# Kernel optimization log

Hardware: AMD Instinct MI355X
Metric: run time of the kernel (lower is better)

## Reference

```python
import jax, jax.numpy as jnp
import numpy as np

B, T, IN = 4, 1024, 172
D, H, FF, L, NCLS = 512, 8, 2048, 8, 1296
HD = D // H
EPS = 1e-5


def setup_inputs() -> dict:
    key = jax.random.key(0)
    ks = jax.random.split(key, 16)
    rn = lambda k, s, sc=0.02: jax.random.normal(k, s, jnp.float32) * sc
    return {
        "poses": jax.random.normal(ks[0], (B, T, IN), jnp.float32),
        "pose_w": rn(ks[1], (D, IN)), "pose_b": jnp.zeros((D,), jnp.float32),
        "in_w": rn(ks[2], (L, 3 * D, D)), "in_b": jnp.zeros((L, 3 * D), jnp.float32),
        "out_w": rn(ks[3], (L, D, D)), "out_b": jnp.zeros((L, D), jnp.float32),
        "ln1_g": jnp.ones((L, D), jnp.float32), "ln1_b": jnp.zeros((L, D), jnp.float32),
        "ffn_w1": rn(ks[4], (L, FF, D)), "ffn_b1": jnp.zeros((L, FF), jnp.float32),
        "ffn_w2": rn(ks[5], (L, D, FF)), "ffn_b2": jnp.zeros((L, D), jnp.float32),
        "ln2_g": jnp.ones((L, D), jnp.float32), "ln2_b": jnp.zeros((L, D), jnp.float32),
        "tcn1_w": rn(ks[6], (512, D, 5)), "tcn1_b": jnp.zeros((512,), jnp.float32),
        "tcn2_w": rn(ks[7], (D, 512, 5)), "tcn2_b": jnp.zeros((D,), jnp.float32),
        "fc1_w": rn(ks[8], (128, D)), "fc1_b": jnp.zeros((128,), jnp.float32),
        "fc2_w": rn(ks[9], (NCLS, 128)), "fc2_b": jnp.zeros((NCLS,), jnp.float32),
    }


def _pos_enc(seq_len, d):
    # PositionalEncoding1D: interleaved sin/cos per frequency pair
    inv_freq = 1.0 / (10000.0 ** (jnp.arange(0, d, 2, dtype=jnp.float32) / d))
    ang = jnp.arange(seq_len, dtype=jnp.float32)[:, None] * inv_freq  # [T, d/2]
    return jnp.stack([jnp.sin(ang), jnp.cos(ang)], axis=-1).reshape(seq_len, d)


def _ln(x, g, b):
    m = x.mean(-1, keepdims=True)
    v = jnp.var(x, axis=-1, keepdims=True)
    return (x - m) * jax.lax.rsqrt(v + EPS) * g + b


def _encoder_layer(x, iw, ib, ow, ob, g1, b1, w1, c1, w2, c2, g2, b2):
    # post-norm TransformerEncoderLayer, eager (non-flash) attention
    Bc, Tc, _ = x.shape
    qkv = x @ iw.T + ib                       # [B,T,3D]
    q, k, v = jnp.split(qkv, 3, axis=-1)
    q = q.reshape(Bc, Tc, H, HD)
    k = k.reshape(Bc, Tc, H, HD)
    v = v.reshape(Bc, Tc, H, HD)
    scores = jnp.einsum('bqhd,bkhd->bhqk', q, k) / jnp.sqrt(jnp.float32(HD))
    attn = jax.nn.softmax(scores, axis=-1)    # explicit weights (need_weights=True)
    o = jnp.einsum('bhqk,bkhd->bqhd', attn, v).reshape(Bc, Tc, D)
    o = o @ ow.T + ob
    x = _ln(x + o, g1, b1)
    f = jax.nn.relu(x @ w1.T + c1) @ w2.T + c2
    return _ln(x + f, g2, b2)


def _conv1d(x, w, b):  # x [B,T,C_in], w [C_out,C_in,5], pad=2
    y = jax.lax.conv_general_dilated(
        x.transpose(0, 2, 1), w, window_strides=(1,), padding=((2, 2),),
        dimension_numbers=('NCH', 'OIH', 'NCH'))
    return y.transpose(0, 2, 1) + b


def _avgpool2(x):  # kernel=2 stride=2 along time
    Bc, Tc, C = x.shape
    return x.reshape(Bc, Tc // 2, 2, C).mean(axis=2)


def reference(poses, pose_w, pose_b, in_w, in_b, out_w, out_b, ln1_g, ln1_b,
              ffn_w1, ffn_b1, ffn_w2, ffn_b2, ln2_g, ln2_b,
              tcn1_w, tcn1_b, tcn2_w, tcn2_b, fc1_w, fc1_b, fc2_w, fc2_b):
    x = poses.reshape(poses.shape[0], poses.shape[1], -1) @ pose_w.T + pose_b
    x = x + _pos_enc(x.shape[1], D)[None]

    def run_stack(h, idx):
        for i in idx:
            h = _encoder_layer(h, in_w[i], in_b[i], out_w[i], out_b[i],
                               ln1_g[i], ln1_b[i], ffn_w1[i], ffn_b1[i],
                               ffn_w2[i], ffn_b2[i], ln2_g[i], ln2_b[i])
        return h

    h = run_stack(x, (0, 1))
    h = run_stack(h, (2, 3)) + h
    h = run_stack(h, (4, 5)) + h
    h = run_stack(h, (6, 7)) + h

    h = _avgpool2(h)                 # [B,T/2,D]
    h = _conv1d(h, tcn1_w, tcn1_b)   # [B,T/2,512]
    h = _avgpool2(h)                 # [B,T/4,512]
    h = _conv1d(h, tcn2_w, tcn2_b)   # [B,T/4,D]
    h = h @ fc1_w.T + fc1_b
    logits = h @ fc2_w.T + fc2_b     # [B,T/4,num_classes]
    return logits
```

## Files before the change

kernel.cpp:

```cpp
#include <hip/hip_runtime.h>
#include <hip/hip_bf16.h>

static constexpr int kB = 4;
static constexpr int kT = 1024;
static constexpr int kIn = 172;
static constexpr int kD = 512;
static constexpr int kH = 8;
static constexpr int kHD = 64;
static constexpr int kFF = 2048;
static constexpr int kNCLS = 1296;
static constexpr float kEps = 1e-5f;

typedef __attribute__((ext_vector_type(8))) short bf16x8_t;
typedef __attribute__((ext_vector_type(4))) float f32x4_t;
typedef __attribute__((ext_vector_type(8))) unsigned short u16x8_t;
typedef __attribute__((ext_vector_type(4))) unsigned short u16x4_t;

static __device__ __forceinline__ unsigned short f2bf(float f) {
  unsigned int u = __float_as_uint(f);
  unsigned int r = (u + 0x7fffu + ((u >> 16) & 1u)) >> 16;
  return (unsigned short)r;
}

__global__ void cvt_kernel(const float* __restrict__ src, ushort* __restrict__ dst, int n8)
{
  const int i = blockIdx.x * 256 + threadIdx.x;
  if (i >= n8) return;
  const float4 a = *(const float4*)&src[i * 8];
  const float4 b = *(const float4*)&src[i * 8 + 4];
  u16x8_t t;
  t[0] = f2bf(a.x); t[1] = f2bf(a.y); t[2] = f2bf(a.z); t[3] = f2bf(a.w);
  t[4] = f2bf(b.x); t[5] = f2bf(b.y); t[6] = f2bf(b.z); t[7] = f2bf(b.w);
  *(u16x8_t*)&dst[i * 8] = t;
}

template<int MR, int NR, int WM, int WN>
__global__ __launch_bounds__(WM * WN * 64) void bgemm_kernel(
    const ushort* __restrict__ A, const ushort* __restrict__ W,
    const float* __restrict__ bias, const float* __restrict__ resid,
    float* __restrict__ C, ushort* __restrict__ Cb, int M, int N, int K, int doRelu)
{
  constexpr int THREADS = WM * WN * 64;
  constexpr int BM = MR * 16 * WM, BN = NR * 16 * WN;
  constexpr int SRD = 72;
  constexpr int TPRA = THREADS / BM, CSA = 64 / TPRA, NLA = CSA / 8;
  constexpr int TPRB = THREADS / BN, CSB = 64 / TPRB, NLB = CSB / 8;
  __shared__ ushort As[BM * SRD];
  __shared__ ushort Bs[BN * SRD];

  const int tid = threadIdx.x;
  int bid = blockIdx.y * gridDim.x + blockIdx.x;
  const int nwg = gridDim.x * gridDim.y;
  if ((nwg & 7) == 0) bid = (bid & 7) * (nwg >> 3) + (bid >> 3);
  const int bm = (bid / gridDim.x) * BM, bn = (bid % gridDim.x) * BN;

  const int wv = tid >> 6, lane = tid & 63;
  const int lr = lane & 15, lg = lane >> 4;
  const int wr = wv / WN, wc = wv % WN;

  const int ra = tid / TPRA, ca = (tid % TPRA) * CSA;
  const int rb = tid / TPRB, cb = (tid % TPRB) * CSB;

  f32x4_t acc[MR][NR];
#pragma unroll
  for (int m = 0; m < MR; ++m)
#pragma unroll
    for (int n = 0; n < NR; ++n) acc[m][n] = (f32x4_t){0.f, 0.f, 0.f, 0.f};

  u16x8_t pa[NLA], pb[NLB];
  auto loadAB = [&](int k0) {
    const ushort* ap = A + (size_t)(bm + ra) * K + k0 + ca;
#pragma unroll
    for (int j = 0; j < NLA; ++j) pa[j] = *(const u16x8_t*)(ap + j * 8);
    const ushort* bp = W + (size_t)(bn + rb) * K + k0 + cb;
#pragma unroll
    for (int j = 0; j < NLB; ++j) pb[j] = *(const u16x8_t*)(bp + j * 8);
  };
  auto storeLDS = [&]() {
#pragma unroll
    for (int j = 0; j < NLA; ++j) *(u16x8_t*)&As[ra * SRD + ca + j * 8] = pa[j];
#pragma unroll
    for (int j = 0; j < NLB; ++j) *(u16x8_t*)&Bs[rb * SRD + cb + j * 8] = pb[j];
  };

  loadAB(0);
  storeLDS();
  __syncthreads();

  const int nsteps = K >> 6;
  for (int s = 0; s < nsteps; ++s) {
    const bool more = (s + 1) < nsteps;
    if (more) loadAB((s + 1) << 6);

#pragma unroll
    for (int kk = 0; kk < 2; ++kk) {
      bf16x8_t af[MR];
#pragma unroll
      for (int m = 0; m < MR; ++m)
        af[m] = *(const bf16x8_t*)&As[(wr * MR * 16 + m * 16 + lr) * SRD + kk * 32 + lg * 8];
#pragma unroll
      for (int n = 0; n < NR; ++n) {
        const bf16x8_t bf = *(const bf16x8_t*)&Bs[(wc * NR * 16 + n * 16 + lr) * SRD + kk * 32 + lg * 8];
#pragma unroll
        for (int m = 0; m < MR; ++m)
          acc[m][n] = __builtin_amdgcn_mfma_f32_16x16x32_bf16(af[m], bf, acc[m][n], 0, 0, 0);
      }
    }
    __syncthreads();
    if (more) { storeLDS(); __syncthreads(); }
  }

#pragma unroll
  for (int m = 0; m < MR; ++m) {
#pragma unroll
    for (int v = 0; v < 4; ++v) {
      const int mm = bm + wr * MR * 16 + m * 16 + lg * 4 + v;
#pragma unroll
      for (int n = 0; n < NR; ++n) {
        const int nn = bn + wc * NR * 16 + n * 16 + lr;
        float val = acc[m][n][v] + bias[nn];
        if (doRelu) val = fmaxf(val, 0.f);
        if (resid) val += resid[(size_t)mm * N + nn];
        if (C)  C[(size_t)mm * N + nn] = val;
        if (Cb) Cb[(size_t)mm * N + nn] = f2bf(val);
      }
    }
  }
}

#define GBM 64
#define GBN 64
#define GBK 16
#define LDST 68

__global__ __launch_bounds__(256) void gemm_kernel(
    const float* __restrict__ A, const float* __restrict__ W,
    const float* __restrict__ bias, const float* __restrict__ resid,
    float* __restrict__ C, int M, int N, int K, int doRelu)
{
  __shared__ __align__(16) float As[GBK][LDST];
  __shared__ __align__(16) float Ws[GBK][LDST];
  const int tid = threadIdx.x;
  const int bm = blockIdx.y * GBM;
  const int bn = blockIdx.x * GBN;
  const int tx = tid & 15, ty = tid >> 4;
  const int li = tid >> 2;
  const int lk = (tid & 3) << 2;

  float acc[4][4];
#pragma unroll
  for (int i = 0; i < 4; ++i)
#pragma unroll
    for (int j = 0; j < 4; ++j) acc[i][j] = 0.f;

  for (int k0 = 0; k0 < K; k0 += GBK) {
    float4 av = make_float4(0.f, 0.f, 0.f, 0.f);
    float4 wv = make_float4(0.f, 0.f, 0.f, 0.f);
    {
      const int m = bm + li;
      if (m < M) {
        if (k0 + lk + 4 <= K) {
          av = *(const float4*)&A[(size_t)m * K + k0 + lk];
        } else {
          float t4[4] = {0.f, 0.f, 0.f, 0.f};
          for (int c = 0; c < 4; ++c) { int k = k0 + lk + c; if (k < K) t4[c] = A[(size_t)m * K + k]; }
          av = make_float4(t4[0], t4[1], t4[2], t4[3]);
        }
      }
      const int n = bn + li;
      if (n < N) {
        if (k0 + lk + 4 <= K) {
          wv = *(const float4*)&W[(size_t)n * K + k0 + lk];
        } else {
          float t4[4] = {0.f, 0.f, 0.f, 0.f};
          for (int c = 0; c < 4; ++c) { int k = k0 + lk + c; if (k < K) t4[c] = W[(size_t)n * K + k]; }
          wv = make_float4(t4[0], t4[1], t4[2], t4[3]);
        }
      }
    }
    __syncthreads();
    As[lk + 0][li] = av.x; As[lk + 1][li] = av.y; As[lk + 2][li] = av.z; As[lk + 3][li] = av.w;
    Ws[lk + 0][li] = wv.x; Ws[lk + 1][li] = wv.y; Ws[lk + 2][li] = wv.z; Ws[lk + 3][li] = wv.w;
    __syncthreads();
#pragma unroll
    for (int kk = 0; kk < GBK; ++kk) {
      const float4 a4 = *(const float4*)&As[kk][ty << 2];
      const float4 b4 = *(const float4*)&Ws[kk][tx << 2];
      const float a[4] = {a4.x, a4.y, a4.z, a4.w};
      const float b[4] = {b4.x, b4.y, b4.z, b4.w};
#pragma unroll
      for (int i = 0; i < 4; ++i)
#pragma unroll
        for (int j = 0; j < 4; ++j) acc[i][j] = fmaf(a[i], b[j], acc[i][j]);
    }
  }

#pragma unroll
  for (int i = 0; i < 4; ++i) {
    const int m = bm + (ty << 2) + i;
    if (m >= M) continue;
#pragma unroll
    for (int j = 0; j < 4; ++j) {
      const int n = bn + (tx << 2) + j;
      if (n >= N) continue;
      float v = acc[i][j] + bias[n];
      if (doRelu) v = fmaxf(v, 0.f);
      if (resid) v += resid[(size_t)m * N + n];
      C[(size_t)m * N + n] = v;
    }
  }
}

__global__ __launch_bounds__(256) void ln_kernel(
    float* __restrict__ X, ushort* __restrict__ Xb,
    const float* __restrict__ g, const float* __restrict__ bta,
    const float* Padd, float* Pout)
{
  const int row = blockIdx.x;
  const int tid = threadIdx.x;
  float* xr = X + (size_t)row * kD;
  const float x0 = xr[tid];
  const float x1 = xr[tid + 256];
  float s = x0 + x1;
  float q = x0 * x0 + x1 * x1;
#pragma unroll
  for (int off = 32; off > 0; off >>= 1) {
    s += __shfl_down(s, off);
    q += __shfl_down(q, off);
  }
  __shared__ float ss[4], qq[4];
  const int w = tid >> 6;
  if ((tid & 63) == 0) { ss[w] = s; qq[w] = q; }
  __syncthreads();
  const float S = ss[0] + ss[1] + ss[2] + ss[3];
  const float Q = qq[0] + qq[1] + qq[2] + qq[3];
  const float mean = S * (1.f / kD);
  const float var = Q * (1.f / kD) - mean * mean;
  const float inv = rsqrtf(var + kEps);
  float v0 = (x0 - mean) * inv * g[tid] + bta[tid];
  float v1 = (x1 - mean) * inv * g[tid + 256] + bta[tid + 256];
  if (Padd) {
    v0 += Padd[(size_t)row * kD + tid];
    v1 += Padd[(size_t)row * kD + tid + 256];
  }
  xr[tid] = v0; xr[tid + 256] = v1;
  ushort* xb = Xb + (size_t)row * kD;
  xb[tid] = f2bf(v0); xb[tid + 256] = f2bf(v1);
  if (Pout) {
    Pout[(size_t)row * kD + tid] = v0;
    Pout[(size_t)row * kD + tid + 256] = v1;
  }
}

#define KSTR 72
#define PSTR 74
__global__ __launch_bounds__(256) void attn_mfma_kernel(
    const ushort* __restrict__ qkv, ushort* __restrict__ O)
{
  const int b = blockIdx.z, h = blockIdx.y;
  const int q0 = blockIdx.x << 6;
  const int tid = threadIdx.x;
  const int wv = tid >> 6, lane = tid & 63;
  const int lr = lane & 15;
  const int lg = lane >> 4;

  __shared__ ushort Ks[64 * KSTR];
  __shared__ ushort Vt[64 * KSTR];
  __shared__ ushort Pl[4][16 * PSTR];

  bf16x8_t qa[2];
  {
    const ushort* qrow = qkv + ((size_t)(b * kT + q0 + wv * 16 + lr)) * (3 * kD) + h * kHD + lg * 8;
    qa[0] = *(const bf16x8_t*)qrow;
    qa[1] = *(const bf16x8_t*)(qrow + 32);
  }

  float m_[4], l_[4];
  f32x4_t oacc[4];
#pragma unroll
  for (int r = 0; r < 4; ++r) { m_[r] = -1e30f; l_[r] = 0.f; }
#pragma unroll
  for (int nb = 0; nb < 4; ++nb) oacc[nb] = (f32x4_t){0.f, 0.f, 0.f, 0.f};

  const int srow = tid >> 2;
  const int sd   = (tid & 3) << 4;
  const int vkp  = tid & 31;
  const int vdh  = tid >> 5;

  u16x8_t k0_, k1_, v0_, v1_;
  auto load_regs = [&](int kt) {
    const ushort* kr = qkv + ((size_t)(b * kT + (kt << 6) + srow)) * (3 * kD) + kD + h * kHD + sd;
    k0_ = *(const u16x8_t*)kr;
    k1_ = *(const u16x8_t*)(kr + 8);
    const ushort* vr = qkv + ((size_t)(b * kT + (kt << 6) + 2 * vkp)) * (3 * kD) + 2 * kD + h * kHD + vdh * 8;
    v0_ = *(const u16x8_t*)vr;
    v1_ = *(const u16x8_t*)(vr + 3 * kD);
  };

  load_regs(0);
  for (int kt = 0; kt < kT / 64; ++kt) {
    __syncthreads();
    {
      *(u16x8_t*)&Ks[srow * KSTR + sd]     = k0_;
      *(u16x8_t*)&Ks[srow * KSTR + sd + 8] = k1_;
#pragma unroll
      for (int e = 0; e < 8; ++e) {
        const unsigned int packv = (unsigned int)v0_[e] | ((unsigned int)v1_[e] << 16);
        *(unsigned int*)&Vt[(vdh * 8 + e) * KSTR + 2 * vkp] = packv;
      }
    }
    __syncthreads();
    if (kt + 1 < kT / 64) load_regs(kt + 1);

    f32x4_t s[4];
#pragma unroll
    for (int cc = 0; cc < 4; ++cc) {
      const ushort* kb = &Ks[(cc * 16 + lr) * KSTR + lg * 8];
      const bf16x8_t kf0 = *(const bf16x8_t*)kb;
      const bf16x8_t kf1 = *(const bf16x8_t*)(kb + 32);
      f32x4_t acc = (f32x4_t){0.f, 0.f, 0.f, 0.f};
      acc = __builtin_amdgcn_mfma_f32_16x16x32_bf16(qa[0], kf0, acc, 0, 0, 0);
      acc = __builtin_amdgcn_mfma_f32_16x16x32_bf16(qa[1], kf1, acc, 0, 0, 0);
#pragma unroll
      for (int r = 0; r < 4; ++r) acc[r] *= 0.125f;
      s[cc] = acc;
    }

#pragma unroll
    for (int r = 0; r < 4; ++r) {
      float mx = fmaxf(fmaxf(s[0][r], s[1][r]), fmaxf(s[2][r], s[3][r]));
      mx = fmaxf(mx, __shfl_xor(mx, 1));
      mx = fmaxf(mx, __shfl_xor(mx, 2));
      mx = fmaxf(mx, __shfl_xor(mx, 4));
      mx = fmaxf(mx, __shfl_xor(mx, 8));
      const float mnew = fmaxf(m_[r], mx);
      const float alpha = __expf(m_[r] - mnew);
      float sum = 0.f;
#pragma unroll
      for (int cc = 0; cc < 4; ++cc) {
        const float p = __expf(s[cc][r] - mnew);
        s[cc][r] = p;
        sum += p;
      }
      sum += __shfl_xor(sum, 1);
      sum += __shfl_xor(sum, 2);
      sum += __shfl_xor(sum, 4);
      sum += __shfl_xor(sum, 8);
      l_[r] = l_[r] * alpha + sum;
      m_[r] = mnew;
#pragma unroll
      for (int nb = 0; nb < 4; ++nb) oacc[nb][r] *= alpha;
#pragma unroll
      for (int cc = 0; cc < 4; ++cc)
        Pl[wv][(lg * 4 + r) * PSTR + cc * 16 + lr] = f2bf(s[cc][r]);
    }

    const bf16x8_t pa0 = *(const bf16x8_t*)&Pl[wv][lr * PSTR + lg * 8];
    const bf16x8_t pa1 = *(const bf16x8_t*)&Pl[wv][lr * PSTR + 32 + lg * 8];
#pragma unroll
    for (int nb = 0; nb < 4; ++nb) {
      const ushort* vb = &Vt[(nb * 16 + lr) * KSTR + lg * 8];
      const bf16x8_t vf0 = *(const bf16x8_t*)vb;
      const bf16x8_t vf1 = *(const bf16x8_t*)(vb + 32);
      oacc[nb] = __builtin_amdgcn_mfma_f32_16x16x32_bf16(pa0, vf0, oacc[nb], 0, 0, 0);
      oacc[nb] = __builtin_amdgcn_mfma_f32_16x16x32_bf16(pa1, vf1, oacc[nb], 0, 0, 0);
    }
  }

#pragma unroll
  for (int nb = 0; nb < 4; ++nb) {
#pragma unroll
    for (int r = 0; r < 4; ++r) {
      const int row = lg * 4 + r;
      const int col = nb * 16 + lr;
      O[((size_t)(b * kT + q0 + wv * 16 + row)) * kD + h * kHD + col] = f2bf(oacc[nb][r] / l_[r]);
    }
  }
}

__global__ __launch_bounds__(256) void posenc_kernel(float* __restrict__ X, ushort* __restrict__ Xb)
{
  const int bt = blockIdx.x;
  const int t = bt & (kT - 1);
  float* row = X + (size_t)bt * kD;
  ushort* rb = Xb + (size_t)bt * kD;
#pragma unroll
  for (int p = 0; p < 2; ++p) {
    const int d = threadIdx.x + p * 256;
    const int j = d >> 1;
    const float inv = expf(-(float)j * 0.03597789207803197f);
    const float ang = (float)t * inv;
    const float pe = (d & 1) ? cosf(ang) : sinf(ang);
    const float v = row[d] + pe;
    row[d] = v;
    rb[d] = f2bf(v);
  }
}

__global__ void im2col_pool_kernel(const float* __restrict__ X, ushort* __restrict__ X5,
                                   int Tt, int n4)
{
  const int idx = blockIdx.x * 256 + threadIdx.x;
  if (idx >= n4) return;
  const int ci4 = idx & 127;
  int r = idx >> 7;
  const int tap = r % 5; r /= 5;
  const int t = r % Tt;
  const int b = r / Tt;
  const int ts = t + tap - 2;
  u16x4_t o = (u16x4_t){0, 0, 0, 0};
  if (ts >= 0 && ts < Tt) {
    const float* p = X + ((size_t)(b * 2 * Tt + 2 * ts)) * kD + ci4 * 4;
    const float4 x0 = *(const float4*)p;
    const float4 x1 = *(const float4*)(p + kD);
    o[0] = f2bf(0.5f * (x0.x + x1.x)); o[1] = f2bf(0.5f * (x0.y + x1.y));
    o[2] = f2bf(0.5f * (x0.z + x1.z)); o[3] = f2bf(0.5f * (x0.w + x1.w));
  }
  *(u16x4_t*)&X5[((size_t)(b * Tt + t)) * 2560 + tap * kD + ci4 * 4] = o;
}

__global__ void convw_t_kernel(const float* __restrict__ w, ushort* __restrict__ Wt)
{
  const int idx = blockIdx.x * 256 + threadIdx.x;
  if (idx >= 512 * 512 * 5) return;
  const int ci = idx & 511;
  int r = idx >> 9;
  const int tap = r % 5;
  const int co = r / 5;
  Wt[(size_t)co * 2560 + tap * 512 + ci] = f2bf(w[(size_t)co * 2560 + ci * 5 + tap]);
}

extern "C" void kernel_launch(void* const* d_in, const int* in_sizes, int n_in,
                              void* d_out, int out_size, void* d_ws, size_t ws_size,
                              hipStream_t stream)
{
  (void)in_sizes; (void)n_in; (void)out_size;
  const float* poses  = (const float*)d_in[0];
  const float* pose_w = (const float*)d_in[1];
  const float* pose_b = (const float*)d_in[2];
  const float* in_w   = (const float*)d_in[3];
  const float* in_b   = (const float*)d_in[4];
  const float* out_w  = (const float*)d_in[5];
  const float* out_b  = (const float*)d_in[6];
  const float* ln1_g  = (const float*)d_in[7];
  const float* ln1_b  = (const float*)d_in[8];
  const float* ffn_w1 = (const float*)d_in[9];
  const float* ffn_b1 = (const float*)d_in[10];
  const float* ffn_w2 = (const float*)d_in[11];
  const float* ffn_b2 = (const float*)d_in[12];
  const float* ln2_g  = (const float*)d_in[13];
  const float* ln2_b  = (const float*)d_in[14];
  const float* tcn1_w = (const float*)d_in[15];
  const float* tcn1_b = (const float*)d_in[16];
  const float* tcn2_w = (const float*)d_in[17];
  const float* tcn2_b = (const float*)d_in[18];
  const float* fc1_w  = (const float*)d_in[19];
  const float* fc1_b  = (const float*)d_in[20];
  const float* fc2_w  = (const float*)d_in[21];
  const float* fc2_b  = (const float*)d_in[22];

  char* base = (char*)d_ws;
  float*  A    = (float*)(base);
  float*  Y    = (float*)(base + 8388608);
  float*  P    = (float*)(base + 16777216);
  ushort* Abf  = (ushort*)(base + 25165824);
  ushort* QKV  = (ushort*)(base + 29360128);
  ushort* Ybf  = QKV;
  ushort* X5   = QKV;
  ushort* MID  = (ushort*)(base + 41943040);
  ushort* ATTb = MID;
  ushort* CW   = MID;
  ushort* Wbf  = (ushort*)(base + 58720256);

  const size_t nWq = (size_t)3 * kD * kD;
  const size_t nWo = (size_t)kD * kD;
  const size_t nW1 = (size_t)kFF * kD;
  const size_t nW2 = (size_t)kD * kFF;
  const size_t nWl = nWq + nWo + nW1 + nW2;
  const bool fullW = ws_size >= (size_t)58720256 + nWl * 8 * 2;

  const int M = kB * kT;
  dim3 blk(256);
  dim3 blk512(512);
  auto cvt = [&](const float* s, ushort* d, size_t n) {
    cvt_kernel<<<(int)((n / 8 + 255) / 256), blk, 0, stream>>>(s, d, (int)(n / 8));
  };

  if (fullW) {
    cvt(in_w,   Wbf,                        nWq * 8);
    cvt(out_w,  Wbf + nWq * 8,              nWo * 8);
    cvt(ffn_w1, Wbf + nWq * 8 + nWo * 8,    nW1 * 8);
    cvt(ffn_w2, Wbf + (nWq + nWo + nW1) * 8, nW2 * 8);
  }

  gemm_kernel<<<dim3(kD / GBN, M / GBM), blk, 0, stream>>>(poses, pose_w, pose_b, nullptr, A, M, kD, kIn, 0);
  posenc_kernel<<<M, blk, 0, stream>>>(A, Abf);

  for (int l = 0; l < 8; ++l) {
    const ushort *Wq, *Wo, *W1, *W2;
    if (fullW) {
      Wq = Wbf + (size_t)l * nWq;
      Wo = Wbf + nWq * 8 + (size_t)l * nWo;
      W1 = Wbf + nWq * 8 + nWo * 8 + (size_t)l * nW1;
      W2 = Wbf + (nWq + nWo + nW1) * 8 + (size_t)l * nW2;
    } else {
      cvt(in_w   + (size_t)l * nWq, Wbf, nWq);
      cvt(out_w  + (size_t)l * nWo, Wbf + nWq, nWo);
      cvt(ffn_w1 + (size_t)l * nW1, Wbf + nWq + nWo, nW1);
      cvt(ffn_w2 + (size_t)l * nW2, Wbf + nWq + nWo + nW1, nW2);
      Wq = Wbf; Wo = Wbf + nWq; W1 = Wbf + nWq + nWo; W2 = Wbf + nWq + nWo + nW1;
    }

    bgemm_kernel<4, 2, 2, 4><<<dim3(3 * kD / 128, M / 128), blk512, 0, stream>>>(
        Abf, Wq, in_b + (size_t)l * 3 * kD, nullptr, nullptr, QKV, M, 3 * kD, kD, 0);
    attn_mfma_kernel<<<dim3(kT / 64, kH, kB), blk, 0, stream>>>(QKV, ATTb);
    bgemm_kernel<2, 2, 4, 2><<<dim3(kD / 64, M / 128), blk512, 0, stream>>>(
        ATTb, Wo, out_b + (size_t)l * kD, A, Y, nullptr, M, kD, kD, 0);
    ln_kernel<<<M, blk, 0, stream>>>(Y, Ybf, ln1_g + (size_t)l * kD, ln1_b + (size_t)l * kD,
                                     nullptr, nullptr);
    bgemm_kernel<4, 2, 2, 4><<<dim3(kFF / 128, M / 128), blk512, 0, stream>>>(
        Ybf, W1, ffn_b1 + (size_t)l * kFF, nullptr, nullptr, MID, M, kFF, kD, 1);
    bgemm_kernel<2, 2, 4, 2><<<dim3(kD / 64, M / 128), blk512, 0, stream>>>(
        MID, W2, ffn_b2 + (size_t)l * kD, Y, A, nullptr, M, kD, kFF, 0);
    {
      const float* padd = (l == 3 || l == 5 || l == 7) ? P : nullptr;
      float* pout = (l == 1 || l == 3 || l == 5) ? P : nullptr;
      ln_kernel<<<M, blk, 0, stream>>>(A, Abf, ln2_g + (size_t)l * kD, ln2_b + (size_t)l * kD,
                                       padd, pout);
    }
  }

  {
    const int T1 = kT / 2;
    const int T2 = kT / 4;
    convw_t_kernel<<<(512 * 512 * 5 + 255) / 256, blk, 0, stream>>>(tcn1_w, CW);
    const int n4a = kB * T1 * 5 * (kD / 4);
    im2col_pool_kernel<<<(n4a + 255) / 256, blk, 0, stream>>>(A, X5, T1, n4a);
    bgemm_kernel<1, 2, 4, 2><<<dim3(kD / 64, kB * T1 / 64), blk512, 0, stream>>>(
        X5, CW, tcn1_b, nullptr, Y, nullptr, kB * T1, kD, 2560, 0);
    convw_t_kernel<<<(512 * 512 * 5 + 255) / 256, blk, 0, stream>>>(tcn2_w, CW);
    const int n4b = kB * T2 * 5 * (kD / 4);
    im2col_pool_kernel<<<(n4b + 255) / 256, blk, 0, stream>>>(Y, X5, T2, n4b);
    bgemm_kernel<1, 2, 4, 2><<<dim3(kD / 64, kB * T2 / 64), blk512, 0, stream>>>(
        X5, CW, tcn2_b, nullptr, A, nullptr, kB * T2, kD, 2560, 0);
    const int Mh = kB * T2;
    gemm_kernel<<<dim3(128 / GBN, Mh / GBM), blk, 0, stream>>>(A, fc1_w, fc1_b, nullptr, Y, Mh, 128, kD, 0);
    gemm_kernel<<<dim3((kNCLS + GBN - 1) / GBN, Mh / GBM), blk, 0, stream>>>(
        Y, fc2_w, fc2_b, nullptr, (float*)d_out, Mh, kNCLS, 128, 0);
  }
}
```

Before: 1.281 ms.

## Double-buffer attention K/V tiles and skip softmax rescale when max barely changes

The attention kernel now keeps two LDS buffers for K and V^T tiles, so only one block barrier is needed per tile and the next tile is written while the current one is consumed. It also adds a lazy online-softmax rescale: the running max and the accumulator rescale are updated only when some row's new max exceeds the old one by more than 8. This removes most exp and multiply work on the accumulators. In exchange, LDS use doubles, which may lower occupancy, and the unnormalized exponentials can grow up to e^8 before a rescale.

```diff
diff --git a/kernel.cpp b/kernel.cpp
--- a/kernel.cpp
+++ b/kernel.cpp
@@ -264,8 +264,8 @@
   const int lr = lane & 15;
   const int lg = lane >> 4;
 
-  __shared__ ushort Ks[64 * KSTR];
-  __shared__ ushort Vt[64 * KSTR];
+  __shared__ ushort Ks[2][64 * KSTR];
+  __shared__ ushort Vt[2][64 * KSTR];
   __shared__ ushort Pl[4][16 * PSTR];
 
   bf16x8_t qa[2];
@@ -287,35 +287,41 @@
   const int vkp  = tid & 31;
   const int vdh  = tid >> 5;
 
+  constexpr int NT = kT / 64;
+  const size_t tstride = (size_t)64 * 3 * kD;
+  const ushort* kptr = qkv + ((size_t)(b * kT + srow)) * (3 * kD) + kD + h * kHD + sd;
+  const ushort* vptr = qkv + ((size_t)(b * kT + 2 * vkp)) * (3 * kD) + 2 * kD + h * kHD + vdh * 8;
+
   u16x8_t k0_, k1_, v0_, v1_;
-  auto load_regs = [&](int kt) {
-    const ushort* kr = qkv + ((size_t)(b * kT + (kt << 6) + srow)) * (3 * kD) + kD + h * kHD + sd;
-    k0_ = *(const u16x8_t*)kr;
-    k1_ = *(const u16x8_t*)(kr + 8);
-    const ushort* vr = qkv + ((size_t)(b * kT + (kt << 6) + 2 * vkp)) * (3 * kD) + 2 * kD + h * kHD + vdh * 8;
-    v0_ = *(const u16x8_t*)vr;
-    v1_ = *(const u16x8_t*)(vr + 3 * kD);
+  auto load_regs = [&]() {
+    k0_ = *(const u16x8_t*)kptr;
+    k1_ = *(const u16x8_t*)(kptr + 8);
+    v0_ = *(const u16x8_t*)vptr;
+    v1_ = *(const u16x8_t*)(vptr + 3 * kD);
+    kptr += tstride; vptr += tstride;
   };
-
-  load_regs(0);
-  for (int kt = 0; kt < kT / 64; ++kt) {
-    __syncthreads();
-    {
-      *(u16x8_t*)&Ks[srow * KSTR + sd]     = k0_;
-      *(u16x8_t*)&Ks[srow * KSTR + sd + 8] = k1_;
-#pragma unroll
-      for (int e = 0; e < 8; ++e) {
-        const unsigned int packv = (unsigned int)v0_[e] | ((unsigned int)v1_[e] << 16);
-        *(unsigned int*)&Vt[(vdh * 8 + e) * KSTR + 2 * vkp] = packv;
-      }
-    }
-    __syncthreads();
-    if (kt + 1 < kT / 64) load_regs(kt + 1);
+  auto write_lds = [&](int buf) {
+    *(u16x8_t*)&Ks[buf][srow * KSTR + sd]     = k0_;
+    *(u16x8_t*)&Ks[buf][srow * KSTR + sd + 8] = k1_;
+#pragma unroll
+    for (int e = 0; e < 8; ++e) {
+      const unsigned int packv = (unsigned int)v0_[e] | ((unsigned int)v1_[e] << 16);
+      *(unsigned int*)&Vt[buf][(vdh * 8 + e) * KSTR + 2 * vkp] = packv;
+    }
+  };
+
+  load_regs();
+  write_lds(0);
+  __syncthreads();
+  load_regs();
+
+  for (int kt = 0; kt < NT; ++kt) {
+    const int buf = kt & 1;
 
     f32x4_t s[4];
 #pragma unroll
     for (int cc = 0; cc < 4; ++cc) {
-      const ushort* kb = &Ks[(cc * 16 + lr) * KSTR + lg * 8];
+      const ushort* kb = &Ks[buf][(cc * 16 + lr) * KSTR + lg * 8];
       const bf16x8_t kf0 = *(const bf16x8_t*)kb;
       const bf16x8_t kf1 = *(const bf16x8_t*)(kb + 32);
       f32x4_t acc = (f32x4_t){0.f, 0.f, 0.f, 0.f};
@@ -326,19 +332,35 @@
       s[cc] = acc;
     }
 
+    float mx[4];
+    int need = 0;
 #pragma unroll
     for (int r = 0; r < 4; ++r) {
-      float mx = fmaxf(fmaxf(s[0][r], s[1][r]), fmaxf(s[2][r], s[3][r]));
-      mx = fmaxf(mx, __shfl_xor(mx, 1));
-      mx = fmaxf(mx, __shfl_xor(mx, 2));
-      mx = fmaxf(mx, __shfl_xor(mx, 4));
-      mx = fmaxf(mx, __shfl_xor(mx, 8));
-      const float mnew = fmaxf(m_[r], mx);
-      const float alpha = __expf(m_[r] - mnew);
+      float m2 = fmaxf(fmaxf(s[0][r], s[1][r]), fmaxf(s[2][r], s[3][r]));
+      m2 = fmaxf(m2, __shfl_xor(m2, 1));
+      m2 = fmaxf(m2, __shfl_xor(m2, 2));
+      m2 = fmaxf(m2, __shfl_xor(m2, 4));
+      m2 = fmaxf(m2, __shfl_xor(m2, 8));
+      mx[r] = m2;
+      if (m2 > m_[r] + 8.f) need = 1;
+    }
+    if (__any(need)) {
+#pragma unroll
+      for (int r = 0; r < 4; ++r) {
+        const float mnew = fmaxf(m_[r], mx[r]);
+        const float alpha = __expf(m_[r] - mnew);
+        l_[r] *= alpha;
+#pragma unroll
+        for (int nb = 0; nb < 4; ++nb) oacc[nb][r] *= alpha;
+        m_[r] = mnew;
+      }
+    }
+#pragma unroll
+    for (int r = 0; r < 4; ++r) {
       float sum = 0.f;
 #pragma unroll
       for (int cc = 0; cc < 4; ++cc) {
-        const float p = __expf(s[cc][r] - mnew);
+        const float p = __expf(s[cc][r] - m_[r]);
         s[cc][r] = p;
         sum += p;
       }
@@ -346,10 +368,7 @@
       sum += __shfl_xor(sum, 2);
       sum += __shfl_xor(sum, 4);
       sum += __shfl_xor(sum, 8);
-      l_[r] = l_[r] * alpha + sum;
-      m_[r] = mnew;
-#pragma unroll
-      for (int nb = 0; nb < 4; ++nb) oacc[nb][r] *= alpha;
+      l_[r] += sum;
 #pragma unroll
       for (int cc = 0; cc < 4; ++cc)
         Pl[wv][(lg * 4 + r) * PSTR + cc * 16 + lr] = f2bf(s[cc][r]);
@@ -359,12 +378,18 @@
     const bf16x8_t pa1 = *(const bf16x8_t*)&Pl[wv][lr * PSTR + 32 + lg * 8];
 #pragma unroll
     for (int nb = 0; nb < 4; ++nb) {
-      const ushort* vb = &Vt[(nb * 16 + lr) * KSTR + lg * 8];
+      const ushort* vb = &Vt[buf][(nb * 16 + lr) * KSTR + lg * 8];
       const bf16x8_t vf0 = *(const bf16x8_t*)vb;
       const bf16x8_t vf1 = *(const bf16x8_t*)(vb + 32);
       oacc[nb] = __builtin_amdgcn_mfma_f32_16x16x32_bf16(pa0, vf0, oacc[nb], 0, 0, 0);
       oacc[nb] = __builtin_amdgcn_mfma_f32_16x16x32_bf16(pa1, vf1, oacc[nb], 0, 0, 0);
     }
+
+    if (kt + 1 < NT) {
+      write_lds(buf ^ 1);
+      if (kt + 2 < NT) load_regs();
+    }
+    __syncthreads();
   }
 
 #pragma unroll
```

Result: no change. 1.262 ms (-1.5%).
